# Optimization experiments

Measured on AMD Instinct MI355X. Metric: run time of the kernel, lower is better.

## Reference

```python
import jax, jax.numpy as jnp
import numpy as np

N, C_IN, C_OUT, H, W = 64, 128, 128, 64, 64
K, RED = 3, 16


def setup_inputs() -> dict:
    key = jax.random.key(0)
    ks = jax.random.split(key, 12)
    s = 0.02
    return {
        "x": jax.random.normal(ks[0], (N, C_IN, H, W), dtype=jnp.float32),
        # spatial_extractor: Linear(16 -> 9)
        "W_sp": jax.random.normal(ks[1], (16, K * K), dtype=jnp.float32) * s,
        "b_sp": jnp.zeros((K * K,), dtype=jnp.float32),
        # out_channel_extractor: Linear(C_IN -> C_OUT//RED) -> ReLU -> Linear(-> C_OUT)
        "W_o1": jax.random.normal(ks[2], (C_IN, C_OUT // RED), dtype=jnp.float32) * s,
        "b_o1": jnp.zeros((C_OUT // RED,), dtype=jnp.float32),
        "W_o2": jax.random.normal(ks[3], (C_OUT // RED, C_OUT), dtype=jnp.float32) * s,
        "b_o2": jnp.zeros((C_OUT,), dtype=jnp.float32),
        # in_channel_extractor: Linear(C_IN -> C_IN//RED) -> ReLU -> Linear(-> C_IN)
        "W_i1": jax.random.normal(ks[4], (C_IN, C_IN // RED), dtype=jnp.float32) * s,
        "b_i1": jnp.zeros((C_IN // RED,), dtype=jnp.float32),
        "W_i2": jax.random.normal(ks[5], (C_IN // RED, C_IN), dtype=jnp.float32) * s,
        "b_i2": jnp.zeros((C_IN,), dtype=jnp.float32),
    }


def reference(x, W_sp, b_sp, W_o1, b_o1, W_o2, b_o2, W_i1, b_i1, W_i2, b_i2):
    n, c, h, w = x.shape
    # AdaptiveAvgPool2d(4): H,W divisible by 4 -> exact 16x16 mean pooling
    xs = x.reshape(n, c, 4, h // 4, 4, w // 4).mean(axis=(3, 5))  # [n,c,4,4]
    xs = xs.reshape(n, c, 16).mean(axis=1)                        # [n,16]
    sp = (xs @ W_sp + b_sp).reshape(n, K, K)                      # [n,3,3]
    gap = x.mean(axis=(2, 3))                                     # [n,C_in]
    co = jax.nn.relu(gap @ W_o1 + b_o1) @ W_o2 + b_o2             # [n,C_out]
    ci = jax.nn.relu(gap @ W_i1 + b_i1) @ W_i2 + b_i2             # [n,C_in]
    # per-sample kernel: [n, C_out, C_in, K, K]
    weight = (co[:, :, None, None, None] * ci[:, None, :, None, None]
              * sp[:, None, None, :, :])

    def per_sample_conv(xi, wi):
        # xi: [C_in,H,W], wi: [C_out,C_in,K,K]
        return jax.lax.conv_general_dilated(
            xi[None], wi, window_strides=(1, 1),
            padding=[(1, 1), (1, 1)])[0]

    return jax.vmap(per_sample_conv)(x, weight)  # [n,C_out,H,W]
```

## Files before the change

### kernel.cpp

```cpp
#include <hip/hip_runtime.h>

#define NB   64
#define CIN  128
#define COUT 128
#define HH   64
#define WW   64
#define HW   4096

typedef float f4v __attribute__((ext_vector_type(4)));


__global__ __launch_bounds__(256) void k_stats(const float* __restrict__ x,
                                               const float* __restrict__ W_i2,
                                               const float* __restrict__ b_i2,
                                               float* __restrict__ bs,
                                               float* __restrict__ B) {
    const int bid = blockIdx.x;
    const int n  = bid >> 2;
    const int rb = bid & 3;
    const int tid = threadIdx.x;
    const int r = tid >> 4;
    const int colq = tid & 15;
    const int y0 = rb * 16;

    __shared__ float lw[9][128];
    __shared__ float bsw[4][4][128];

    if (tid < 128) {
        lw[8][tid] = b_i2[tid];
        #pragma unroll
        for (int j = 0; j < 8; ++j) lw[j][tid] = W_i2[j * CIN + tid];
    }
    __syncthreads();

    float4 acc[9];
    #pragma unroll
    for (int j = 0; j < 9; ++j) acc[j] = make_float4(0.f, 0.f, 0.f, 0.f);

    const size_t xbase = (size_t)n * CIN * HW + (size_t)(y0 + r) * WW + colq * 4;
    const int wv = tid >> 6;
    const int cb = colq >> 2;
    const bool rep = (tid & 0x33) == 0;

    for (int c = 0; c < 128; ++c) {
        f4v v = __builtin_nontemporal_load((const f4v*)(x + xbase + (size_t)c * HW));
        #pragma unroll
        for (int j = 0; j < 9; ++j) {
            const float w = lw[j][c];
            acc[j].x += w * v.x; acc[j].y += w * v.y;
            acc[j].z += w * v.z; acc[j].w += w * v.w;
        }
        float ls = (v.x + v.y) + (v.z + v.w);
        ls += __shfl_xor(ls, 1,  64);
        ls += __shfl_xor(ls, 2,  64);
        ls += __shfl_xor(ls, 16, 64);
        ls += __shfl_xor(ls, 32, 64);
        if (rep) bsw[wv][cb][c] = ls;
    }
    __syncthreads();

    #pragma unroll
    for (int k = 0; k < 2; ++k) {
        const int idx = tid + 256 * k;
        const int c = idx >> 2, cb2 = idx & 3;
        const float s = bsw[0][cb2][c] + bsw[1][cb2][c] + bsw[2][cb2][c] + bsw[3][cb2][c];
        bs[((size_t)n * CIN + c) * 16 + rb * 4 + cb2] = s;
    }

    const size_t bpix = (size_t)(y0 + r) * WW + colq * 4;
    #pragma unroll
    for (int j = 0; j < 9; ++j) {
        *(float4*)(B + ((size_t)j * NB + n) * HW + bpix) = acc[j];
    }
}

__global__ __launch_bounds__(256) void k_out(
    const float* __restrict__ B, const float* __restrict__ bs,
    const float* __restrict__ W_sp, const float* __restrict__ b_sp,
    const float* __restrict__ W_o1, const float* __restrict__ b_o1,
    const float* __restrict__ W_o2, const float* __restrict__ b_o2,
    const float* __restrict__ W_i1, const float* __restrict__ b_i1,
    float* __restrict__ out)
{
    const int bid = blockIdx.x;
    const int n  = bid >> 3;
    const int y0 = (bid & 7) * 8;
    const int tid = threadIdx.x;

    __shared__ float lbs[128][17];
    __shared__ float lgap[128];
    __shared__ float lxsm[16];
    __shared__ float lh[16];
    __shared__ float lco[128];
    __shared__ float lsp[9];
    __shared__ float ts[10][66];

    if (tid < 128) {
        const int c = tid;
        const float* src = bs + ((size_t)n * CIN + c) * 16;
        float s = 0.0f;
        #pragma unroll
        for (int j = 0; j < 16; ++j) { const float v = src[j]; lbs[c][j] = v; s += v; }
        lgap[c] = s * (1.0f / 4096.0f);
    }
    __syncthreads();

    if (tid < 16) {
        float acc = 0.0f;
        for (int i = 0; i < 128; ++i) acc += lbs[i][tid];
        lxsm[tid] = acc * (1.0f / 32768.0f);
    }
    if (tid < 8) {
        float acc = b_o1[tid];
        for (int i = 0; i < 128; ++i) acc += lgap[i] * W_o1[i * 8 + tid];
        lh[tid] = fmaxf(acc, 0.0f);
    } else if (tid < 16) {
        const int j = tid - 8;
        float acc = b_i1[j];
        for (int i = 0; i < 128; ++i) acc += lgap[i] * W_i1[i * 8 + j];
        lh[tid] = fmaxf(acc, 0.0f);
    }
    __syncthreads();

    if (tid < 128) {
        float acco = b_o2[tid];
        #pragma unroll
        for (int j = 0; j < 8; ++j) acco += lh[j] * W_o2[j * 128 + tid];
        lco[tid] = acco;
    }
    if (tid < 9) {
        float acc = b_sp[tid];
        #pragma unroll
        for (int j = 0; j < 16; ++j) acc += lxsm[j] * W_sp[j * 9 + tid];
        lsp[tid] = acc;
    }
    __syncthreads();

    if (tid < 160) {
        const int ry = tid >> 4, cq = tid & 15;
        const int gy = y0 - 1 + ry;
        float4 tv = make_float4(0.f, 0.f, 0.f, 0.f);
        if (gy >= 0 && gy < HH) {
            const size_t pix = (size_t)gy * WW + cq * 4;
            const float* Bn = B + (size_t)n * HW + pix;
            float4 a = *(const float4*)(Bn + (size_t)8 * NB * HW);
            tv = a;
            #pragma unroll
            for (int j = 0; j < 8; ++j) {
                const float h = lh[8 + j];
                float4 u = *(const float4*)(Bn + (size_t)j * NB * HW);
                tv.x += h * u.x; tv.y += h * u.y;
                tv.z += h * u.z; tv.w += h * u.w;
            }
        }
        ts[ry][cq * 4 + 0] = tv.x; ts[ry][cq * 4 + 1] = tv.y;
        ts[ry][cq * 4 + 2] = tv.z; ts[ry][cq * 4 + 3] = tv.w;
    }
    __syncthreads();

    const int i = tid & 127;
    const int row = i >> 4;
    const int cc0 = (i & 15) * 4;
    float sv[4];
    #pragma unroll
    for (int u = 0; u < 4; ++u) {
        const int cc = cc0 + u;
        float acc = 0.0f;
        #pragma unroll
        for (int dy = 0; dy < 3; ++dy) {
            #pragma unroll
            for (int dx = 0; dx < 3; ++dx) {
                const int cx = cc + dx - 1;
                if (cx >= 0 && cx < WW)
                    acc += lsp[dy * 3 + dx] * ts[row + dy][cx];
            }
        }
        sv[u] = acc;
    }

    const int ohalf = (tid >> 7) * 64;
    float* outp = out + (size_t)n * COUT * HW + (size_t)y0 * WW + (size_t)i * 4;
    #pragma unroll 4
    for (int op = 0; op < 64; ++op) {
        const int o = ohalf + op;
        const float scl = lco[o];
        f4v v; v.x = sv[0] * scl; v.y = sv[1] * scl; v.z = sv[2] * scl; v.w = sv[3] * scl;
        __builtin_nontemporal_store(v, (f4v*)(outp + (size_t)o * HW));
    }
}

extern "C" void kernel_launch(void* const* d_in, const int* in_sizes, int n_in,
                              void* d_out, int out_size, void* d_ws, size_t ws_size,
                              hipStream_t stream) {
    const float* x    = (const float*)d_in[0];
    const float* W_sp = (const float*)d_in[1];
    const float* b_sp = (const float*)d_in[2];
    const float* W_o1 = (const float*)d_in[3];
    const float* b_o1 = (const float*)d_in[4];
    const float* W_o2 = (const float*)d_in[5];
    const float* b_o2 = (const float*)d_in[6];
    const float* W_i1 = (const float*)d_in[7];
    const float* b_i1 = (const float*)d_in[8];
    const float* W_i2 = (const float*)d_in[9];
    const float* b_i2 = (const float*)d_in[10];

    float* ws = (float*)d_ws;
    float* bs = ws;
    float* B  = ws + 147456;
    float* out = (float*)d_out;

    k_stats<<<NB * 4, 256, 0, stream>>>(x, W_i2, b_i2, bs, B);
    k_out<<<NB * 8, 256, 0, stream>>>(B, bs, W_sp, b_sp, W_o1, b_o1,
                                      W_o2, b_o2, W_i1, b_i1, out);
}
```

Baseline: 318.4 us.

## Split k_stats channel loop across two thread halves and pre-reduce pooled stats

k_stats now launches 512 blocks of 8 rows each. Each block splits the 128 input channels into two 64-channel halves handled by separate groups of 128 threads. The partial projection accumulators are combined through shared memory before B is stored. Per-block channel sums and 4x4 pooled sums are pre-reduced into compact gapp/xsmp buffers, so k_out reads fewer values and does less reduction work. The intent is more parallelism and a shorter serial channel loop per thread, at the cost of extra shared memory and a second barrier.

```diff
diff --git a/kernel.cpp b/kernel.cpp
--- a/kernel.cpp
+++ b/kernel.cpp
@@ -13,23 +13,28 @@
 __global__ __launch_bounds__(256) void k_stats(const float* __restrict__ x,
                                                const float* __restrict__ W_i2,
                                                const float* __restrict__ b_i2,
-                                               float* __restrict__ bs,
+                                               float* __restrict__ gapp,
+                                               float* __restrict__ xsmp,
                                                float* __restrict__ B) {
     const int bid = blockIdx.x;
-    const int n  = bid >> 2;
-    const int rb = bid & 3;
+    const int n  = bid >> 3;
+    const int rt = bid & 7;
     const int tid = threadIdx.x;
-    const int r = tid >> 4;
-    const int colq = tid & 15;
-    const int y0 = rb * 16;
-
-    __shared__ float lw[9][128];
-    __shared__ float bsw[4][4][128];
-
-    if (tid < 128) {
-        lw[8][tid] = b_i2[tid];
-        #pragma unroll
-        for (int j = 0; j < 8; ++j) lw[j][tid] = W_i2[j * CIN + tid];
+    const int cs = tid >> 7;
+    const int p  = tid & 127;
+    const int row = p >> 4;
+    const int colq = p & 15;
+    const int wv = tid >> 6;
+    const int cb = colq >> 2;
+
+    __shared__ float lw[2][9][64];
+    __shared__ float bsw[4][4][72];
+    __shared__ float cacc[9][4][128];
+
+    for (int k = tid; k < 1152; k += 256) {
+        const int half = k / 576, jj = (k % 576) >> 6, c = k & 63;
+        lw[half][jj][c] = (jj == 8) ? b_i2[half * 64 + c]
+                                    : W_i2[jj * CIN + half * 64 + c];
     }
     __syncthreads();
 
@@ -37,16 +42,16 @@
     #pragma unroll
     for (int j = 0; j < 9; ++j) acc[j] = make_float4(0.f, 0.f, 0.f, 0.f);
 
-    const size_t xbase = (size_t)n * CIN * HW + (size_t)(y0 + r) * WW + colq * 4;
-    const int wv = tid >> 6;
-    const int cb = colq >> 2;
+    const size_t xbase = ((size_t)n * CIN + cs * 64) * HW
+                       + (size_t)(rt * 8 + row) * WW + colq * 4;
     const bool rep = (tid & 0x33) == 0;
 
-    for (int c = 0; c < 128; ++c) {
+    #pragma unroll 4
+    for (int c = 0; c < 64; ++c) {
         f4v v = __builtin_nontemporal_load((const f4v*)(x + xbase + (size_t)c * HW));
         #pragma unroll
         for (int j = 0; j < 9; ++j) {
-            const float w = lw[j][c];
+            const float w = lw[cs][j][c];
             acc[j].x += w * v.x; acc[j].y += w * v.y;
             acc[j].z += w * v.z; acc[j].w += w * v.w;
         }
@@ -59,23 +64,53 @@
     }
     __syncthreads();
 
-    #pragma unroll
-    for (int k = 0; k < 2; ++k) {
-        const int idx = tid + 256 * k;
-        const int c = idx >> 2, cb2 = idx & 3;
-        const float s = bsw[0][cb2][c] + bsw[1][cb2][c] + bsw[2][cb2][c] + bsw[3][cb2][c];
-        bs[((size_t)n * CIN + c) * 16 + rb * 4 + cb2] = s;
-    }
-
-    const size_t bpix = (size_t)(y0 + r) * WW + colq * 4;
-    #pragma unroll
-    for (int j = 0; j < 9; ++j) {
-        *(float4*)(B + ((size_t)j * NB + n) * HW + bpix) = acc[j];
+    if (cs == 1) {
+        #pragma unroll
+        for (int j = 0; j < 9; ++j) {
+            cacc[j][0][p] = acc[j].x; cacc[j][1][p] = acc[j].y;
+            cacc[j][2][p] = acc[j].z; cacc[j][3][p] = acc[j].w;
+        }
+    }
+
+    if (tid < 128) {
+        const int half = tid >> 6, c = tid & 63;
+        float s = 0.0f;
+        #pragma unroll
+        for (int q = 0; q < 4; ++q)
+            s += bsw[half * 2][q][c] + bsw[half * 2 + 1][q][c];
+        gapp[((size_t)n * 8 + rt) * 128 + half * 64 + c] = s;
+    }
+    {
+        const int colb = wv, c = tid & 63;
+        float s2 = bsw[0][colb][c] + bsw[1][colb][c]
+                 + bsw[2][colb][c] + bsw[3][colb][c];
+        s2 += __shfl_xor(s2, 1,  64);
+        s2 += __shfl_xor(s2, 2,  64);
+        s2 += __shfl_xor(s2, 4,  64);
+        s2 += __shfl_xor(s2, 8,  64);
+        s2 += __shfl_xor(s2, 16, 64);
+        s2 += __shfl_xor(s2, 32, 64);
+        if (c == 0) xsmp[((size_t)n * 8 + rt) * 4 + colb] = s2;
+    }
+    __syncthreads();
+
+    if (cs == 0) {
+        const size_t bpix = (size_t)(rt * 8 + row) * WW + colq * 4;
+        #pragma unroll
+        for (int j = 0; j < 9; ++j) {
+            f4v v;
+            v.x = acc[j].x + cacc[j][0][p];
+            v.y = acc[j].y + cacc[j][1][p];
+            v.z = acc[j].z + cacc[j][2][p];
+            v.w = acc[j].w + cacc[j][3][p];
+            __builtin_nontemporal_store(v, (f4v*)(B + ((size_t)j * NB + n) * HW + bpix));
+        }
     }
 }
 
 __global__ __launch_bounds__(256) void k_out(
-    const float* __restrict__ B, const float* __restrict__ bs,
+    const float* __restrict__ B,
+    const float* __restrict__ gapp, const float* __restrict__ xsmp,
     const float* __restrict__ W_sp, const float* __restrict__ b_sp,
     const float* __restrict__ W_o1, const float* __restrict__ b_o1,
     const float* __restrict__ W_o2, const float* __restrict__ b_o2,
@@ -87,7 +122,6 @@
     const int y0 = (bid & 7) * 8;
     const int tid = threadIdx.x;
 
-    __shared__ float lbs[128][17];
     __shared__ float lgap[128];
     __shared__ float lxsm[16];
     __shared__ float lh[16];
@@ -96,20 +130,20 @@
     __shared__ float ts[10][66];
 
     if (tid < 128) {
-        const int c = tid;
-        const float* src = bs + ((size_t)n * CIN + c) * 16;
         float s = 0.0f;
         #pragma unroll
-        for (int j = 0; j < 16; ++j) { const float v = src[j]; lbs[c][j] = v; s += v; }
-        lgap[c] = s * (1.0f / 4096.0f);
-    }
-    __syncthreads();
-
+        for (int rt = 0; rt < 8; ++rt)
+            s += gapp[((size_t)n * 8 + rt) * 128 + tid];
+        lgap[tid] = s * (1.0f / 4096.0f);
+    }
     if (tid < 16) {
-        float acc = 0.0f;
-        for (int i = 0; i < 128; ++i) acc += lbs[i][tid];
-        lxsm[tid] = acc * (1.0f / 32768.0f);
-    }
+        const int rowblk = tid >> 2, colb = tid & 3;
+        const float s = xsmp[((size_t)n * 8 + rowblk * 2) * 4 + colb]
+                      + xsmp[((size_t)n * 8 + rowblk * 2 + 1) * 4 + colb];
+        lxsm[tid] = s * (1.0f / 32768.0f);
+    }
+    __syncthreads();
+
     if (tid < 8) {
         float acc = b_o1[tid];
         for (int i = 0; i < 128; ++i) acc += lgap[i] * W_o1[i * 8 + tid];
@@ -205,11 +239,12 @@
     const float* b_i2 = (const float*)d_in[10];
 
     float* ws = (float*)d_ws;
-    float* bs = ws;
-    float* B  = ws + 147456;
-    float* out = (float*)d_out;
-
-    k_stats<<<NB * 4, 256, 0, stream>>>(x, W_i2, b_i2, bs, B);
-    k_out<<<NB * 8, 256, 0, stream>>>(B, bs, W_sp, b_sp, W_o1, b_o1,
+    float* gapp = ws;
+    float* xsmp = ws + 65536;
+    float* B    = ws + 73728;
+    float* out  = (float*)d_out;
+
+    k_stats<<<NB * 8, 256, 0, stream>>>(x, W_i2, b_i2, gapp, xsmp, B);
+    k_out<<<NB * 8, 256, 0, stream>>>(B, gapp, xsmp, W_sp, b_sp, W_o1, b_o1,
                                       W_o2, b_o2, W_i1, b_i1, out);
 }
```

New measurement: 281.5 us. 1.13x faster.
